# Performance work log

Measured on AMD Instinct MI355X. Metric: run time of the kernel, lower is better.

Reference implementation:

```python
import math
import jax, jax.numpy as jnp
import numpy as np

D_MODEL = 768
D_CROSS = 768
D_HEAD = 64
N_HEADS = D_MODEL // D_HEAD  # 12
D_FF = D_MODEL * 3           # 2304
EPS = 1e-6
N_FREQ = D_HEAD // 8         # freqs per axis (3 axes -> theta dim 24, rotates first 48 of 64 dims)


def make_rope_freqs():
    # k-diffusion style geometric frequencies in [pi, 10*pi), one table shared per head
    n = N_HEADS * N_FREQ
    f = np.exp(np.linspace(math.log(math.pi), math.log(10.0 * math.pi), n + 1)[:-1])
    return jnp.asarray(f.reshape(N_FREQ, N_HEADS).T, dtype=jnp.float32)  # [nh, N_FREQ]

ROPE_FREQS = make_rope_freqs()


def rms_norm(x, scale):
    ms = jnp.mean(jnp.square(x), axis=-1, keepdims=True)
    return x * (scale * jax.lax.rsqrt(ms + EPS))


def cos_scale(q, k, scale):
    # cosine-sim QK rescale: unit-normalize q,k per head then multiply by sqrt(learned scale)
    s = jnp.sqrt(scale)[:, None, None]  # [nh,1,1]
    q = q * (s * jax.lax.rsqrt(jnp.sum(jnp.square(q), -1, keepdims=True) + EPS))
    k = k * (s * jax.lax.rsqrt(jnp.sum(jnp.square(k), -1, keepdims=True) + EPS))
    return q, k


def rope_theta(pos):
    # pos [b,l,3] -> theta [b,nh,l,3*N_FREQ]
    b, l, _ = pos.shape
    th = pos[..., None, :, None] * ROPE_FREQS[:, None, :]  # [b,l,nh,3,N_FREQ]
    th = th.reshape(b, l, N_HEADS, 3 * N_FREQ)
    return jnp.swapaxes(th, 1, 2)  # movedim(-2,-3)


def apply_rope(x, theta):
    d = theta.shape[-1]
    x1, x2, x3 = x[..., :d], x[..., d:2 * d], x[..., 2 * d:]
    c, s = jnp.cos(theta), jnp.sin(theta)
    return jnp.concatenate([x1 * c - x2 * s, x2 * c + x1 * s, x3], axis=-1)


def sdpa(q, k, v):
    # scale=1.0 (cosine-sim already scaled)
    a = jax.nn.softmax(jnp.einsum('bhqe,bhke->bhqk', q, k), axis=-1)
    return jnp.einsum('bhqk,bhke->bhqe', a, v)


def reference(x, pos, x_cross, pos_cross,
              sa_norm_scale, sa_wqkv, sa_scale, sa_wout,
              ca_norm_scale, ca_norm_cross_scale, ca_wq, ca_wkv, ca_scale, ca_wout,
              ff_norm_scale, ff_wup, ff_wdown):
    b, l, _ = x.shape
    lc = x_cross.shape[1]

    # --- self attention ---
    h = rms_norm(x, sa_norm_scale)
    qkv = (h @ sa_wqkv.T).reshape(b, l, 3, N_HEADS, D_HEAD).transpose(2, 0, 3, 1, 4)
    q, k, v = qkv[0], qkv[1], qkv[2]  # [b,nh,l,e]
    q, k = cos_scale(q, k, sa_scale)
    theta = rope_theta(pos)
    q = apply_rope(q, theta)
    k = apply_rope(k, theta)
    o = sdpa(q, k, v)
    o = jnp.swapaxes(o, 1, 2).reshape(b, l, D_MODEL)
    x = o @ sa_wout.T + x

    # --- cross attention ---
    h = rms_norm(x, ca_norm_scale)
    hc = rms_norm(x_cross, ca_norm_cross_scale)
    q = (h @ ca_wq.T).reshape(b, l, N_HEADS, D_HEAD).transpose(0, 2, 1, 3)
    kv = (hc @ ca_wkv.T).reshape(b, lc, 2, N_HEADS, D_HEAD).transpose(2, 0, 3, 1, 4)
    k, v = kv[0], kv[1]
    q, k = cos_scale(q, k, ca_scale)
    q = apply_rope(q, rope_theta(pos))
    k = apply_rope(k, rope_theta(pos_cross))
    o = sdpa(q, k, v)
    o = jnp.swapaxes(o, 1, 2).reshape(b, l, D_MODEL)
    x = o @ ca_wout.T + x

    # --- SwiGLU FFN ---
    u = rms_norm(x, ff_norm_scale) @ ff_wup.T  # [b,l,2*d_ff]
    a, g = jnp.split(u, 2, axis=-1)
    x = (a * jax.nn.silu(g)) @ ff_wdown.T + x
    return x


def setup_inputs() -> dict:
    key = jax.random.key(0)
    ks = jax.random.split(key, 16)
    B, L = 2, 2048

    def w(k, out_f, in_f):
        return jax.random.normal(k, (out_f, in_f), dtype=jnp.float32) * (1.0 / math.sqrt(in_f))

    return {
        'x': jax.random.normal(ks[0], (B, L, D_MODEL), dtype=jnp.float32),
        'pos': jax.random.uniform(ks[1], (B, L, 3), dtype=jnp.float32),
        'x_cross': jax.random.normal(ks[2], (B, L, D_CROSS), dtype=jnp.float32),
        'pos_cross': jax.random.uniform(ks[3], (B, L, 3), dtype=jnp.float32),
        'sa_norm_scale': jnp.ones((D_MODEL,), jnp.float32),
        'sa_wqkv': w(ks[4], 3 * D_MODEL, D_MODEL),
        'sa_scale': jnp.full((N_HEADS,), 10.0, jnp.float32),
        'sa_wout': w(ks[5], D_MODEL, D_MODEL) * 0.02,
        'ca_norm_scale': jnp.ones((D_MODEL,), jnp.float32),
        'ca_norm_cross_scale': jnp.ones((D_CROSS,), jnp.float32),
        'ca_wq': w(ks[6], D_MODEL, D_MODEL),
        'ca_wkv': w(ks[7], 2 * D_MODEL, D_CROSS),
        'ca_scale': jnp.full((N_HEADS,), 10.0, jnp.float32),
        'ca_wout': w(ks[8], D_MODEL, D_MODEL) * 0.02,
        'ff_norm_scale': jnp.ones((D_MODEL,), jnp.float32),
        'ff_wup': w(ks[9], 2 * D_FF, D_MODEL),
        'ff_wdown': w(ks[10], D_MODEL, D_FF) * 0.02,
    }
```

## Files before the change

### kernel.cpp

```cpp
#include <hip/hip_runtime.h>
#include <hip/hip_bf16.h>
#include <math.h>

typedef __hip_bfloat16 bf16;

#define B 2
#define L 2048
#define DM 768
#define NH 12
#define DH 64
#define DFF 2304
#define M_TOK (B * L)

typedef __attribute__((ext_vector_type(8))) short bfrag;
typedef __attribute__((ext_vector_type(4))) float ffrag;
typedef __attribute__((ext_vector_type(16))) float facc16;

__device__ __forceinline__ float waveSum(float v) {
#pragma unroll
  for (int o = 32; o > 0; o >>= 1) v += __shfl_down(v, o, 64);
  return v;
}

__device__ __forceinline__ void gld16(void* l, const void* g) {
  __builtin_amdgcn_global_load_lds((const __attribute__((address_space(1))) unsigned*)g,
                                   (__attribute__((address_space(3))) unsigned*)l, 16, 0, 0);
}

#define BAR1_N(N) do { asm volatile("s_waitcnt vmcnt(" #N ")" ::: "memory"); \
                       __builtin_amdgcn_s_barrier(); } while (0)
#define BAR2() do { asm volatile("s_waitcnt lgkmcnt(0)" ::: "memory"); \
                    __builtin_amdgcn_s_barrier(); } while (0)

#define ASW(row, chunk) (((row) << 6) + ((((chunk) ^ ((row)&7))) << 3))

__global__ void k_castall(const float* __restrict__ s0, const float* __restrict__ s1,
                          const float* __restrict__ s2, const float* __restrict__ s3,
                          const float* __restrict__ s4, const float* __restrict__ s5,
                          const float* __restrict__ s6, bf16* __restrict__ dst) {
  const size_t DM2 = (size_t)DM * DM;
  size_t u = ((size_t)blockIdx.x * 256 + threadIdx.x) * 4;
  if (u >= 17 * DM2) return;
  const float* src;
  size_t loc;
  if (u < 3 * DM2) { src = s0; loc = u; }
  else if (u < 4 * DM2) { src = s1; loc = u - 3 * DM2; }
  else if (u < 5 * DM2) { src = s2; loc = u - 4 * DM2; }
  else if (u < 7 * DM2) { src = s3; loc = u - 5 * DM2; }
  else if (u < 8 * DM2) { src = s4; loc = u - 7 * DM2; }
  else if (u < 14 * DM2) { src = s5; loc = u - 8 * DM2; }
  else { src = s6; loc = u - 14 * DM2; }
  float4 v = *(const float4*)&src[loc];
  bf16* d = dst + u;
  d[0] = __float2bfloat16(v.x);
  d[1] = __float2bfloat16(v.y);
  d[2] = __float2bfloat16(v.z);
  d[3] = __float2bfloat16(v.w);
}

__global__ __launch_bounds__(256) void k_rmsnorm(const float* __restrict__ in,
                                                 const float* __restrict__ scale,
                                                 bf16* __restrict__ out) {
  int row = blockIdx.x;
  int t = threadIdx.x;
  const float* r = in + (size_t)row * DM;
  float x0 = r[t], x1 = r[t + 256], x2 = r[t + 512];
  float ss = x0 * x0 + x1 * x1 + x2 * x2;
  ss = waveSum(ss);
  __shared__ float red[4];
  int w = t >> 6, ln = t & 63;
  if (ln == 0) red[w] = ss;
  __syncthreads();
  float tot = red[0] + red[1] + red[2] + red[3];
  float g = rsqrtf(tot / (float)DM + 1e-6f);
  bf16* o = out + (size_t)row * DM;
  o[t] = __float2bfloat16(x0 * g * scale[t]);
  o[t + 256] = __float2bfloat16(x1 * g * scale[t + 256]);
  o[t + 512] = __float2bfloat16(x2 * g * scale[t + 512]);
}

template <int NT, int OBF>
__global__ __launch_bounds__(256) void k_gemm(const bf16* __restrict__ A,
                                              const bf16* __restrict__ W,
                                              float* __restrict__ C,
                                              bf16* __restrict__ Cb,
                                              const float* __restrict__ res,
                                              int M, int N, int K) {
  __shared__ __align__(16) bf16 As[2 * 128 * 32];
  __shared__ __align__(16) bf16 Bs[2 * NT * 32];
  const int t = threadIdx.x;
  const int w = t >> 6, lane = t & 63;
  const int m0 = blockIdx.y * 128, n0 = blockIdx.x * NT;
  const int quad = lane >> 4, l16 = lane & 15;
  constexpr int MI = (NT == 128) ? 4 : 2;
  const int wrow = (NT == 128) ? (w >> 1) * 64 : w * 32;
  const int wcol = (NT == 128) ? (w & 1) * 64 : 0;

  ffrag acc[MI][4];
#pragma unroll
  for (int i = 0; i < MI; i++)
#pragma unroll
    for (int j = 0; j < 4; j++) acc[i][j] = (ffrag){0.f, 0.f, 0.f, 0.f};

  auto stage = [&](int k0, int sel) {
#pragma unroll
    for (int it = 0; it < 2; it++) {
      int lc = (w * 2 + it) * 64 + lane;
      int row = lc >> 2;
      int kc = (lc & 3) ^ ((row >> 1) & 3);
      gld16(&As[sel * 4096 + lc * 8], &A[(size_t)(m0 + row) * K + k0 + kc * 8]);
    }
    if (NT == 128) {
#pragma unroll
      for (int it = 0; it < 2; it++) {
        int lc = (w * 2 + it) * 64 + lane;
        int row = lc >> 2;
        int kc = (lc & 3) ^ ((row >> 1) & 3);
        gld16(&Bs[sel * 4096 + lc * 8], &W[(size_t)(n0 + row) * K + k0 + kc * 8]);
      }
    } else {
      int lc = w * 64 + lane;
      int row = lc >> 2;
      int kc = (lc & 3) ^ ((row >> 1) & 3);
      gld16(&Bs[sel * 2048 + lc * 8], &W[(size_t)(n0 + row) * K + k0 + kc * 8]);
    }
  };

  const int NK = K >> 5;
  stage(0, 0);
  for (int kt = 0; kt < NK; kt++) {
    int cur = kt & 1;
    if (kt + 1 < NK) {
      stage((kt + 1) * 32, cur ^ 1);
      if constexpr (NT == 128) BAR1_N(4); else BAR1_N(3);
    } else {
      BAR1_N(0);
    }
    const bf16* Ab = As + cur * 4096;
    const bf16* Bb = Bs + cur * (NT == 128 ? 4096 : 2048);
    bfrag af[MI], bfv[4];
#pragma unroll
    for (int i = 0; i < MI; i++) {
      int r = wrow + i * 16 + l16;
      af[i] = *(const bfrag*)&Ab[r * 32 + (quad ^ ((r >> 1) & 3)) * 8];
    }
#pragma unroll
    for (int j = 0; j < 4; j++) {
      int r = wcol + j * 16 + l16;
      bfv[j] = *(const bfrag*)&Bb[r * 32 + (quad ^ ((r >> 1) & 3)) * 8];
    }
#pragma unroll
    for (int i = 0; i < MI; i++)
#pragma unroll
      for (int j = 0; j < 4; j++)
        acc[i][j] = __builtin_amdgcn_mfma_f32_16x16x32_bf16(af[i], bfv[j], acc[i][j], 0, 0, 0);
    BAR2();
  }
#pragma unroll
  for (int i = 0; i < MI; i++) {
    int mrow = m0 + wrow + i * 16 + quad * 4;
#pragma unroll
    for (int j = 0; j < 4; j++) {
      int ncol = n0 + wcol + j * 16 + l16;
#pragma unroll
      for (int r = 0; r < 4; r++) {
        float v = acc[i][j][r];
        size_t idx = (size_t)(mrow + r) * N + ncol;
        if (OBF) {
          Cb[idx] = __float2bfloat16(v);
        } else {
          if (res) v += res[idx];
          C[idx] = v;
        }
      }
    }
  }
}

__global__ __launch_bounds__(256) void k_ffup(const bf16* __restrict__ A,
                                              const bf16* __restrict__ Wup,
                                              bf16* __restrict__ Out) {
  __shared__ __align__(16) bf16 As[2 * 128 * 32];
  __shared__ __align__(16) bf16 Ba[2 * 64 * 32];
  __shared__ __align__(16) bf16 Bg[2 * 64 * 32];
  const int t = threadIdx.x, w = t >> 6, lane = t & 63;
  const int m0 = blockIdx.y * 128, n0 = blockIdx.x * 64;
  const int quad = lane >> 4, l16 = lane & 15;

  ffrag aa[2][4], ag[2][4];
#pragma unroll
  for (int i = 0; i < 2; i++)
#pragma unroll
    for (int j = 0; j < 4; j++) {
      aa[i][j] = (ffrag){0.f, 0.f, 0.f, 0.f};
      ag[i][j] = (ffrag){0.f, 0.f, 0.f, 0.f};
    }

  auto stage = [&](int k0, int sel) {
#pragma unroll
    for (int it = 0; it < 2; it++) {
      int lc = (w * 2 + it) * 64 + lane;
      int row = lc >> 2;
      int kc = (lc & 3) ^ ((row >> 1) & 3);
      gld16(&As[sel * 4096 + lc * 8], &A[(size_t)(m0 + row) * DM + k0 + kc * 8]);
    }
    {
      int lc = w * 64 + lane;
      int row = lc >> 2;
      int kc = (lc & 3) ^ ((row >> 1) & 3);
      gld16(&Ba[sel * 2048 + lc * 8], &Wup[(size_t)(n0 + row) * DM + k0 + kc * 8]);
      gld16(&Bg[sel * 2048 + lc * 8], &Wup[(size_t)(DFF + n0 + row) * DM + k0 + kc * 8]);
    }
  };

  const int NK = DM / 32;
  stage(0, 0);
  for (int kt = 0; kt < NK; kt++) {
    int cur = kt & 1;
    if (kt + 1 < NK) {
      stage((kt + 1) * 32, cur ^ 1);
      BAR1_N(4);
    } else {
      BAR1_N(0);
    }
    const bf16* Ab = As + cur * 4096;
    const bf16* Bab = Ba + cur * 2048;
    const bf16* Bgb = Bg + cur * 2048;
    bfrag af[2], ba[4], bg[4];
#pragma unroll
    for (int i = 0; i < 2; i++) {
      int r = w * 32 + i * 16 + l16;
      af[i] = *(const bfrag*)&Ab[r * 32 + (quad ^ ((r >> 1) & 3)) * 8];
    }
#pragma unroll
    for (int j = 0; j < 4; j++) {
      int r = j * 16 + l16;
      int sw = (quad ^ ((r >> 1) & 3)) * 8;
      ba[j] = *(const bfrag*)&Bab[r * 32 + sw];
      bg[j] = *(const bfrag*)&Bgb[r * 32 + sw];
    }
#pragma unroll
    for (int i = 0; i < 2; i++)
#pragma unroll
      for (int j = 0; j < 4; j++) {
        aa[i][j] = __builtin_amdgcn_mfma_f32_16x16x32_bf16(af[i], ba[j], aa[i][j], 0, 0, 0);
        ag[i][j] = __builtin_amdgcn_mfma_f32_16x16x32_bf16(af[i], bg[j], ag[i][j], 0, 0, 0);
      }
    BAR2();
  }
#pragma unroll
  for (int i = 0; i < 2; i++) {
    int mrow = m0 + w * 32 + i * 16 + quad * 4;
#pragma unroll
    for (int j = 0; j < 4; j++) {
      int ncol = n0 + j * 16 + l16;
#pragma unroll
      for (int r = 0; r < 4; r++) {
        float a = aa[i][j][r], g = ag[i][j][r];
        float v = a * g / (1.f + __expf(-g));
        Out[(size_t)(mrow + r) * DFF + ncol] = __float2bfloat16(v);
      }
    }
  }
}

__device__ __forceinline__ float rope_apply(float x, const float* __restrict__ pos3, float s,
                                            int h, int lane) {
  float ss = x * x;
#pragma unroll
  for (int m = 32; m > 0; m >>= 1) ss += __shfl_xor(ss, m, 64);
  x *= s * rsqrtf(ss + 1e-6f);
  int j = lane < 24 ? lane : (lane < 48 ? lane - 24 : 0);
  int partner = lane < 24 ? lane + 24 : (lane < 48 ? lane - 24 : lane);
  float other = __shfl(x, partner, 64);
  if (lane < 48) {
    int c = j >> 3, f = j & 7;
    float fr = __expf(1.14472988584940017f +
                      (float)(f * 12 + h) * (2.30258509299404568f / 96.0f));
    float th = pos3[c] * fr;
    float st = __sinf(th), ct = __cosf(th);
    return (lane < 24) ? (x * ct - other * st) : (x * ct + other * st);
  }
  return x;
}

__global__ __launch_bounds__(256) void k_ropeqk(const bf16* __restrict__ inQ, int strQ, int offQ,
                                                const bf16* __restrict__ inK, int strK, int offK,
                                                const float* __restrict__ posQ,
                                                const float* __restrict__ posK,
                                                const float* __restrict__ scale,
                                                bf16* __restrict__ outQ, bf16* __restrict__ outK) {
  int item = blockIdx.x * 4 + (threadIdx.x >> 6);
  int lane = threadIdx.x & 63;
  int l = item % L;
  int bh = item / L;
  int h = bh % NH;
  int b = bh / NH;
  float s = sqrtf(scale[h]);
  size_t tokrow = (size_t)(b * L + l);
  float xq = __bfloat162float(inQ[tokrow * strQ + offQ + h * DH + lane]);
  float oq = rope_apply(xq, &posQ[tokrow * 3], s, h, lane);
  outQ[(size_t)item * DH + lane] = __float2bfloat16(oq);
  float xk = __bfloat162float(inK[tokrow * strK + offK + h * DH + lane]);
  float ok = rope_apply(xk, &posK[tokrow * 3], s, h, lane);
  outK[(size_t)item * DH + lane] = __float2bfloat16(ok);
}

__global__ __launch_bounds__(256) void k_vtrans(const bf16* __restrict__ in, int stride, int off,
                                                bf16* __restrict__ Vt) {
  __shared__ __align__(16) bf16 St[64 * 64];
  int lt = blockIdx.x & 31, bh = blockIdx.x >> 5;
  int h = bh % NH, b = bh / NH;
  int t = threadIdx.x;
#pragma unroll
  for (int pass = 0; pass < 2; pass++) {
    int cid = t + pass * 256;
    int r = cid >> 3, c = cid & 7;
    *(float4*)&St[ASW(r, c)] =
        *(const float4*)&in[(size_t)(b * L + lt * 64 + r) * stride + off + h * DH + c * 8];
  }
  __syncthreads();
  const short* Ss = (const short*)St;
#pragma unroll
  for (int pass = 0; pass < 2; pass++) {
    int cid = t + pass * 256;
    int d = cid >> 3, oc = cid & 7;
    bfrag tmp;
#pragma unroll
    for (int i = 0; i < 8; i++) {
      int p = oc * 8 + i;
      int tok = (p & ~12) | ((p & 4) << 1) | ((p & 8) >> 1);
      tmp[i] = Ss[(tok << 6) + ((((d >> 3) ^ (tok & 7))) << 3) + (d & 7)];
    }
    *(bfrag*)&Vt[((size_t)bh * DH + d) * L + lt * 64 + oc * 8] = tmp;
  }
}

__global__ __launch_bounds__(256) void k_attn_mfma(const bf16* __restrict__ Q,
                                                   const bf16* __restrict__ K,
                                                   const bf16* __restrict__ Vt,
                                                   const float* __restrict__ scale,
                                                   bf16* __restrict__ O) {
  __shared__ __align__(16) char smem[32768 + 512];
  bf16* Ks = (bf16*)smem;
  bf16* Vs = (bf16*)(smem + 16384);
  float* Oex = (float*)smem;
  float* Lred = (float*)(smem + 32768);
  int qt = blockIdx.x & 31, bh = blockIdx.x >> 5;
  int h = bh % NH, b = bh / NH;
  float smax = scale[h];
  float nsl2 = -smax * 1.442695040888963f;
  int t = threadIdx.x, w = t >> 6, lane = t & 63;
  int hh = lane >> 5, l32 = lane & 31;
  int qsub = w >> 1, ksub = w & 1;

  const bf16* kbase = K + (size_t)(bh * L) * DH;
  const bf16* vbase = Vt + (size_t)bh * DH * L;

  const bf16* qrow = Q + ((size_t)(bh * L) + qt * 64 + qsub * 32 + l32) * DH;
  bfrag qf[4];
#pragma unroll
  for (int c = 0; c < 4; c++) qf[c] = *(const bfrag*)&qrow[c * 16 + hh * 8];

  facc16 o0, o1;
#pragma unroll
  for (int i = 0; i < 16; i++) { o0[i] = 0.f; o1[i] = 0.f; }
  float l_run = 0.f;

  auto stageKV = [&](int kt, int sel) {
    int k0 = kt * 64;
    bf16* Kb = Ks + sel * 4096;
    bf16* Vb = Vs + sel * 4096;
#pragma unroll
    for (int h2 = 0; h2 < 2; h2++) {
      int r = w * 8 + (lane >> 3) + h2 * 32;
      int kc = (lane & 7) ^ (r & 7);
      int ldsrow = (w * 8 + h2 * 32) * 64;
      gld16(&Kb[ldsrow + lane * 8], &kbase[(size_t)(k0 + r) * DH + kc * 8]);
      gld16(&Vb[ldsrow + lane * 8], &vbase[(size_t)r * L + k0 + kc * 8]);
    }
  };

  stageKV(0, 0);
  for (int kt = 0; kt < 32; kt++) {
    int cur = kt & 1;
    if (kt < 31) {
      stageKV(kt + 1, cur ^ 1);
      BAR1_N(4);
    } else {
      BAR1_N(0);
    }
    const bf16* Kb = Ks + cur * 4096;
    const bf16* Vb = Vs + cur * 4096;
    facc16 s;
#pragma unroll
    for (int i = 0; i < 16; i++) s[i] = 0.f;
#pragma unroll
    for (int c = 0; c < 4; c++) {
      bfrag kf = *(const bfrag*)&Kb[ASW(ksub * 32 + l32, c * 2 + hh)];
      s = __builtin_amdgcn_mfma_f32_32x32x16_bf16(kf, qf[c], s, 0, 0, 0);
    }
    float pv[16];
#pragma unroll
    for (int reg = 0; reg < 16; reg++) {
      float p = __builtin_amdgcn_exp2f(__builtin_fmaf(s[reg], 1.442695040888963f, nsl2));
      l_run += p;
      pv[reg] = p;
    }
    bfrag pf0, pf1;
#pragma unroll
    for (int j = 0; j < 8; j++) {
      pf0[j] = __builtin_bit_cast(short, __float2bfloat16(pv[j]));
      pf1[j] = __builtin_bit_cast(short, __float2bfloat16(pv[8 + j]));
    }
    {
      bfrag vf;
      vf = *(const bfrag*)&Vb[ASW(l32, ksub * 4 + hh)];
      o0 = __builtin_amdgcn_mfma_f32_32x32x16_bf16(pf0, vf, o0, 0, 0, 0);
      vf = *(const bfrag*)&Vb[ASW(l32, ksub * 4 + 2 + hh)];
      o0 = __builtin_amdgcn_mfma_f32_32x32x16_bf16(pf1, vf, o0, 0, 0, 0);
      vf = *(const bfrag*)&Vb[ASW(32 + l32, ksub * 4 + hh)];
      o1 = __builtin_amdgcn_mfma_f32_32x32x16_bf16(pf0, vf, o1, 0, 0, 0);
      vf = *(const bfrag*)&Vb[ASW(32 + l32, ksub * 4 + 2 + hh)];
      o1 = __builtin_amdgcn_mfma_f32_32x32x16_bf16(pf1, vf, o1, 0, 0, 0);
    }
    BAR2();
  }
  l_run += __shfl_xor(l_run, 32, 64);
  __syncthreads();
  {
    int gd = (ksub ^ 1) * 32 + l32;
#pragma unroll
    for (int reg = 0; reg < 16; reg++) {
      int row = (reg & 3) + 8 * (reg >> 2) + 4 * hh;
      float gv = ksub ? o0[reg] : o1[reg];
      Oex[(size_t)(qsub * 32 + row) * 64 + gd] = gv;
    }
  }
  if (lane < 32) Lred[ksub * 64 + qsub * 32 + lane] = l_run;
  __syncthreads();
  {
    int d = ksub * 32 + l32;
#pragma unroll
    for (int reg = 0; reg < 16; reg++) {
      int row = (reg & 3) + 8 * (reg >> 2) + 4 * hh;
      int qg2 = qsub * 32 + row;
      float ltot = Lred[qg2] + Lred[64 + qg2];
      float keep = ksub ? o1[reg] : o0[reg];
      float v = (keep + Oex[(size_t)qg2 * 64 + d]) / ltot;
      O[(((size_t)(b * L) + qt * 64 + qg2) * NH + h) * DH + d] = __float2bfloat16(v);
    }
  }
}

extern "C" void kernel_launch(void* const* d_in, const int* in_sizes, int n_in,
                              void* d_out, int out_size, void* d_ws, size_t ws_size,
                              hipStream_t stream) {
  const float* x = (const float*)d_in[0];
  const float* pos = (const float*)d_in[1];
  const float* x_cross = (const float*)d_in[2];
  const float* pos_cross = (const float*)d_in[3];
  const float* sa_norm_scale = (const float*)d_in[4];
  const float* sa_wqkv = (const float*)d_in[5];
  const float* sa_scale = (const float*)d_in[6];
  const float* sa_wout = (const float*)d_in[7];
  const float* ca_norm_scale = (const float*)d_in[8];
  const float* ca_norm_cross_scale = (const float*)d_in[9];
  const float* ca_wq = (const float*)d_in[10];
  const float* ca_wkv = (const float*)d_in[11];
  const float* ca_scale = (const float*)d_in[12];
  const float* ca_wout = (const float*)d_in[13];
  const float* ff_norm_scale = (const float*)d_in[14];
  const float* ff_wup = (const float*)d_in[15];
  const float* ff_wdown = (const float*)d_in[16];
  float* out = (float*)d_out;

  float* ws = (float*)d_ws;
  const size_t S = (size_t)M_TOK * DM;
  float* xbuf = ws;
  bf16* b16 = (bf16*)(ws + S);
  bf16* qkvb = b16;
  bf16* qb = b16 + 3 * S;
  bf16* kb = b16 + 4 * S;
  bf16* vtb = b16 + 5 * S;
  bf16* hb = b16 + 6 * S;
  bf16* hcb = b16 + 7 * S;
  bf16* obb = b16 + 8 * S;
  bf16* wqkvb = b16 + 9 * S;
  bf16* woutb = wqkvb + (size_t)3 * DM * DM;
  bf16* wqb = woutb + (size_t)DM * DM;
  bf16* wkvb = wqb + (size_t)DM * DM;
  bf16* wout2b = wkvb + (size_t)2 * DM * DM;
  bf16* wupb = wout2b + (size_t)DM * DM;
  bf16* wdownb = wupb + (size_t)2 * DFF * DM;
  bf16* ffb = qkvb;

  const int ropeGrid = B * NH * L / 4;
  const int attnGrid = B * NH * (L / 64);
  const int vtGrid = B * NH * (L / 64);
  const size_t DM2 = (size_t)DM * DM;
  const int castGrid = (int)((17 * DM2 / 4 + 255) / 256);

  k_castall<<<castGrid, 256, 0, stream>>>(sa_wqkv, sa_wout, ca_wq, ca_wkv, ca_wout, ff_wup,
                                          ff_wdown, wqkvb);

  k_rmsnorm<<<M_TOK, 256, 0, stream>>>(x_cross, ca_norm_cross_scale, hcb);

  k_rmsnorm<<<M_TOK, 256, 0, stream>>>(x, sa_norm_scale, hb);
  k_gemm<128, 1><<<dim3(3 * DM / 128, M_TOK / 128), 256, 0, stream>>>(
      hb, wqkvb, nullptr, qkvb, nullptr, M_TOK, 3 * DM, DM);
  k_ropeqk<<<ropeGrid, 256, 0, stream>>>(qkvb, 3 * DM, 0, qkvb, 3 * DM, DM, pos, pos, sa_scale,
                                         qb, kb);
  k_vtrans<<<vtGrid, 256, 0, stream>>>(qkvb, 3 * DM, 2 * DM, vtb);
  k_attn_mfma<<<attnGrid, 256, 0, stream>>>(qb, kb, vtb, sa_scale, obb);
  k_gemm<64, 0><<<dim3(DM / 64, M_TOK / 128), 256, 0, stream>>>(
      obb, woutb, xbuf, nullptr, x, M_TOK, DM, DM);

  k_rmsnorm<<<M_TOK, 256, 0, stream>>>(xbuf, ca_norm_scale, hb);
  k_gemm<64, 1><<<dim3(DM / 64, M_TOK / 128), 256, 0, stream>>>(
      hb, wqb, nullptr, qkvb, nullptr, M_TOK, DM, DM);
  k_gemm<128, 1><<<dim3(2 * DM / 128, M_TOK / 128), 256, 0, stream>>>(
      hcb, wkvb, nullptr, qkvb + S, nullptr, M_TOK, 2 * DM, DM);
  k_ropeqk<<<ropeGrid, 256, 0, stream>>>(qkvb, DM, 0, qkvb + S, 2 * DM, 0, pos, pos_cross,
                                         ca_scale, qb, kb);
  k_vtrans<<<vtGrid, 256, 0, stream>>>(qkvb + S, 2 * DM, DM, vtb);
  k_attn_mfma<<<attnGrid, 256, 0, stream>>>(qb, kb, vtb, ca_scale, obb);
  k_gemm<64, 0><<<dim3(DM / 64, M_TOK / 128), 256, 0, stream>>>(
      obb, wout2b, xbuf, nullptr, xbuf, M_TOK, DM, DM);

  k_rmsnorm<<<M_TOK, 256, 0, stream>>>(xbuf, ff_norm_scale, hb);
  k_ffup<<<dim3(DFF / 64, M_TOK / 128), 256, 0, stream>>>(hb, wupb, ffb);
  k_gemm<64, 0><<<dim3(DM / 64, M_TOK / 128), 256, 0, stream>>>(
      ffb, wdownb, out, nullptr, xbuf, M_TOK, DM, DFF);
}
```

Baseline: 459.5 us.

## Vectorize RoPE to 8 lanes per head row and precompute load pointers

The RoPE/cos-scale kernel now processes each head row with 8 lanes handling 8 bf16 elements each, using 128-bit loads and stores and a 3-step shuffle reduction. Per-element exp-based frequencies are replaced by a geometric recurrence, and the grid shrinks 8x. Separately, the GEMM, SwiGLU GEMM and attention staging lambdas precompute global pointers and LDS offsets once and advance the pointers each k-step, cutting per-iteration address arithmetic. The frequency recurrence can accumulate small rounding differences compared with computing each frequency directly.

```diff
diff --git a/kernel.cpp b/kernel.cpp
--- a/kernel.cpp
+++ b/kernel.cpp
@@ -102,36 +102,41 @@
 #pragma unroll
     for (int j = 0; j < 4; j++) acc[i][j] = (ffrag){0.f, 0.f, 0.f, 0.f};
 
-  auto stage = [&](int k0, int sel) {
-#pragma unroll
-    for (int it = 0; it < 2; it++) {
-      int lc = (w * 2 + it) * 64 + lane;
-      int row = lc >> 2;
-      int kc = (lc & 3) ^ ((row >> 1) & 3);
-      gld16(&As[sel * 4096 + lc * 8], &A[(size_t)(m0 + row) * K + k0 + kc * 8]);
-    }
+  const bf16 *pA0, *pA1, *pB0, *pB1 = nullptr;
+  int lA0, lA1, lB0, lB1 = 0;
+  {
+    int lc0 = (w * 2 + 0) * 64 + lane;
+    int r0 = lc0 >> 2, kc0 = (lc0 & 3) ^ ((r0 >> 1) & 3);
+    int lc1 = (w * 2 + 1) * 64 + lane;
+    int r1 = lc1 >> 2, kc1 = (lc1 & 3) ^ ((r1 >> 1) & 3);
+    pA0 = A + (size_t)(m0 + r0) * K + kc0 * 8; lA0 = lc0 * 8;
+    pA1 = A + (size_t)(m0 + r1) * K + kc1 * 8; lA1 = lc1 * 8;
     if (NT == 128) {
-#pragma unroll
-      for (int it = 0; it < 2; it++) {
-        int lc = (w * 2 + it) * 64 + lane;
-        int row = lc >> 2;
-        int kc = (lc & 3) ^ ((row >> 1) & 3);
-        gld16(&Bs[sel * 4096 + lc * 8], &W[(size_t)(n0 + row) * K + k0 + kc * 8]);
-      }
+      pB0 = W + (size_t)(n0 + r0) * K + kc0 * 8; lB0 = lc0 * 8;
+      pB1 = W + (size_t)(n0 + r1) * K + kc1 * 8; lB1 = lc1 * 8;
     } else {
       int lc = w * 64 + lane;
-      int row = lc >> 2;
-      int kc = (lc & 3) ^ ((row >> 1) & 3);
-      gld16(&Bs[sel * 2048 + lc * 8], &W[(size_t)(n0 + row) * K + k0 + kc * 8]);
+      int r = lc >> 2, kc = (lc & 3) ^ ((r >> 1) & 3);
+      pB0 = W + (size_t)(n0 + r) * K + kc * 8; lB0 = lc * 8;
+    }
+  }
+  auto stage = [&](int sel) {
+    gld16(&As[sel * 4096 + lA0], pA0); pA0 += 32;
+    gld16(&As[sel * 4096 + lA1], pA1); pA1 += 32;
+    if (NT == 128) {
+      gld16(&Bs[sel * 4096 + lB0], pB0); pB0 += 32;
+      gld16(&Bs[sel * 4096 + lB1], pB1); pB1 += 32;
+    } else {
+      gld16(&Bs[sel * 2048 + lB0], pB0); pB0 += 32;
     }
   };
 
   const int NK = K >> 5;
-  stage(0, 0);
+  stage(0);
   for (int kt = 0; kt < NK; kt++) {
     int cur = kt & 1;
     if (kt + 1 < NK) {
-      stage((kt + 1) * 32, cur ^ 1);
+      stage(cur ^ 1);
       if constexpr (NT == 128) BAR1_N(4); else BAR1_N(3);
     } else {
       BAR1_N(0);
@@ -196,29 +201,34 @@
       ag[i][j] = (ffrag){0.f, 0.f, 0.f, 0.f};
     }
 
-  auto stage = [&](int k0, int sel) {
-#pragma unroll
-    for (int it = 0; it < 2; it++) {
-      int lc = (w * 2 + it) * 64 + lane;
-      int row = lc >> 2;
-      int kc = (lc & 3) ^ ((row >> 1) & 3);
-      gld16(&As[sel * 4096 + lc * 8], &A[(size_t)(m0 + row) * DM + k0 + kc * 8]);
-    }
-    {
-      int lc = w * 64 + lane;
-      int row = lc >> 2;
-      int kc = (lc & 3) ^ ((row >> 1) & 3);
-      gld16(&Ba[sel * 2048 + lc * 8], &Wup[(size_t)(n0 + row) * DM + k0 + kc * 8]);
-      gld16(&Bg[sel * 2048 + lc * 8], &Wup[(size_t)(DFF + n0 + row) * DM + k0 + kc * 8]);
-    }
+  const bf16 *pA0, *pA1, *pBa, *pBg;
+  int lA0, lA1, lBc;
+  {
+    int lc0 = (w * 2 + 0) * 64 + lane;
+    int r0 = lc0 >> 2, kc0 = (lc0 & 3) ^ ((r0 >> 1) & 3);
+    int lc1 = (w * 2 + 1) * 64 + lane;
+    int r1 = lc1 >> 2, kc1 = (lc1 & 3) ^ ((r1 >> 1) & 3);
+    pA0 = A + (size_t)(m0 + r0) * DM + kc0 * 8; lA0 = lc0 * 8;
+    pA1 = A + (size_t)(m0 + r1) * DM + kc1 * 8; lA1 = lc1 * 8;
+    int lc = w * 64 + lane;
+    int r = lc >> 2, kc = (lc & 3) ^ ((r >> 1) & 3);
+    pBa = Wup + (size_t)(n0 + r) * DM + kc * 8;
+    pBg = Wup + (size_t)(DFF + n0 + r) * DM + kc * 8;
+    lBc = lc * 8;
+  }
+  auto stage = [&](int sel) {
+    gld16(&As[sel * 4096 + lA0], pA0); pA0 += 32;
+    gld16(&As[sel * 4096 + lA1], pA1); pA1 += 32;
+    gld16(&Ba[sel * 2048 + lBc], pBa); pBa += 32;
+    gld16(&Bg[sel * 2048 + lBc], pBg); pBg += 32;
   };
 
   const int NK = DM / 32;
-  stage(0, 0);
+  stage(0);
   for (int kt = 0; kt < NK; kt++) {
     int cur = kt & 1;
     if (kt + 1 < NK) {
-      stage((kt + 1) * 32, cur ^ 1);
+      stage(cur ^ 1);
       BAR1_N(4);
     } else {
       BAR1_N(0);
@@ -264,24 +274,45 @@
   }
 }
 
-__device__ __forceinline__ float rope_apply(float x, const float* __restrict__ pos3, float s,
-                                            int h, int lane) {
-  float ss = x * x;
-#pragma unroll
-  for (int m = 32; m > 0; m >>= 1) ss += __shfl_xor(ss, m, 64);
-  x *= s * rsqrtf(ss + 1e-6f);
-  int j = lane < 24 ? lane : (lane < 48 ? lane - 24 : 0);
-  int partner = lane < 24 ? lane + 24 : (lane < 48 ? lane - 24 : lane);
-  float other = __shfl(x, partner, 64);
-  if (lane < 48) {
-    int c = j >> 3, f = j & 7;
-    float fr = __expf(1.14472988584940017f +
-                      (float)(f * 12 + h) * (2.30258509299404568f / 96.0f));
-    float th = pos3[c] * fr;
-    float st = __sinf(th), ct = __cosf(th);
-    return (lane < 24) ? (x * ct - other * st) : (x * ct + other * st);
-  }
-  return x;
+__device__ __forceinline__ void rope8(const bf16* __restrict__ inp, const float* __restrict__ pos3,
+                                      float s, float fr0, int k, int lane,
+                                      bf16* __restrict__ outp) {
+  bfrag v = *(const bfrag*)inp;
+  float x[8];
+#pragma unroll
+  for (int i = 0; i < 8; i++) x[i] = __bfloat162float(__builtin_bit_cast(bf16, (short)v[i]));
+  float ss = 0.f;
+#pragma unroll
+  for (int i = 0; i < 8; i++) ss += x[i] * x[i];
+  ss += __shfl_xor(ss, 1, 64);
+  ss += __shfl_xor(ss, 2, 64);
+  ss += __shfl_xor(ss, 4, 64);
+  float g = s * rsqrtf(ss + 1e-6f);
+#pragma unroll
+  for (int i = 0; i < 8; i++) x[i] *= g;
+  int pk = k < 3 ? k + 3 : (k < 6 ? k - 3 : k);
+  int psrc = (lane & 56) | pk;
+  float other[8];
+#pragma unroll
+  for (int i = 0; i < 8; i++) other[i] = __shfl(x[i], psrc, 64);
+  bfrag o;
+  if (k < 6) {
+    int c = k < 3 ? k : k - 3;
+    float p = pos3[c];
+    float fr = fr0;
+    float sgn = k < 3 ? -1.f : 1.f;
+#pragma unroll
+    for (int i = 0; i < 8; i++) {
+      float th = p * fr;
+      fr *= 1.333521432163324f;
+      float st = __sinf(th), ct = __cosf(th);
+      o[i] = __builtin_bit_cast(short, __float2bfloat16(x[i] * ct + sgn * other[i] * st));
+    }
+  } else {
+#pragma unroll
+    for (int i = 0; i < 8; i++) o[i] = __builtin_bit_cast(short, __float2bfloat16(x[i]));
+  }
+  *(bfrag*)outp = o;
 }
 
 __global__ __launch_bounds__(256) void k_ropeqk(const bf16* __restrict__ inQ, int strQ, int offQ,
@@ -290,20 +321,21 @@
                                                 const float* __restrict__ posK,
                                                 const float* __restrict__ scale,
                                                 bf16* __restrict__ outQ, bf16* __restrict__ outK) {
-  int item = blockIdx.x * 4 + (threadIdx.x >> 6);
+  int wid = blockIdx.x * 4 + (threadIdx.x >> 6);
   int lane = threadIdx.x & 63;
+  int k = lane & 7;
+  int item = wid * 8 + (lane >> 3);
   int l = item % L;
   int bh = item / L;
   int h = bh % NH;
   int b = bh / NH;
   float s = sqrtf(scale[h]);
+  float fr0 = __expf(1.14472988584940017f + (float)h * 0.023985261385354646f);
   size_t tokrow = (size_t)(b * L + l);
-  float xq = __bfloat162float(inQ[tokrow * strQ + offQ + h * DH + lane]);
-  float oq = rope_apply(xq, &posQ[tokrow * 3], s, h, lane);
-  outQ[(size_t)item * DH + lane] = __float2bfloat16(oq);
-  float xk = __bfloat162float(inK[tokrow * strK + offK + h * DH + lane]);
-  float ok = rope_apply(xk, &posK[tokrow * 3], s, h, lane);
-  outK[(size_t)item * DH + lane] = __float2bfloat16(ok);
+  rope8(inQ + tokrow * strQ + offQ + h * DH + k * 8, &posQ[tokrow * 3], s, fr0, k, lane,
+        outQ + (size_t)item * DH + k * 8);
+  rope8(inK + tokrow * strK + offK + h * DH + k * 8, &posK[tokrow * 3], s, fr0, k, lane,
+        outK + (size_t)item * DH + k * 8);
 }
 
 __global__ __launch_bounds__(256) void k_vtrans(const bf16* __restrict__ in, int stride, int off,
@@ -367,25 +399,32 @@
   for (int i = 0; i < 16; i++) { o0[i] = 0.f; o1[i] = 0.f; }
   float l_run = 0.f;
 
-  auto stageKV = [&](int kt, int sel) {
-    int k0 = kt * 64;
-    bf16* Kb = Ks + sel * 4096;
-    bf16* Vb = Vs + sel * 4096;
-#pragma unroll
-    for (int h2 = 0; h2 < 2; h2++) {
-      int r = w * 8 + (lane >> 3) + h2 * 32;
-      int kc = (lane & 7) ^ (r & 7);
-      int ldsrow = (w * 8 + h2 * 32) * 64;
-      gld16(&Kb[ldsrow + lane * 8], &kbase[(size_t)(k0 + r) * DH + kc * 8]);
-      gld16(&Vb[ldsrow + lane * 8], &vbase[(size_t)r * L + k0 + kc * 8]);
-    }
+  const bf16 *kg0, *kg1, *vg0, *vg1;
+  int lk0, lk1;
+  {
+    int r0 = w * 8 + (lane >> 3);
+    int kc0 = (lane & 7) ^ (r0 & 7);
+    int r1 = r0 + 32;
+    int kc1 = (lane & 7) ^ (r1 & 7);
+    kg0 = kbase + (size_t)r0 * DH + kc0 * 8;
+    kg1 = kbase + (size_t)r1 * DH + kc1 * 8;
+    vg0 = vbase + (size_t)r0 * L + kc0 * 8;
+    vg1 = vbase + (size_t)r1 * L + kc1 * 8;
+    lk0 = (w * 8) * 64 + lane * 8;
+    lk1 = (w * 8 + 32) * 64 + lane * 8;
+  }
+  auto stageKV = [&](int sel) {
+    gld16(&Ks[sel * 4096 + lk0], kg0); kg0 += 64 * DH;
+    gld16(&Ks[sel * 4096 + lk1], kg1); kg1 += 64 * DH;
+    gld16(&Vs[sel * 4096 + lk0], vg0); vg0 += 64;
+    gld16(&Vs[sel * 4096 + lk1], vg1); vg1 += 64;
   };
 
-  stageKV(0, 0);
+  stageKV(0);
   for (int kt = 0; kt < 32; kt++) {
     int cur = kt & 1;
     if (kt < 31) {
-      stageKV(kt + 1, cur ^ 1);
+      stageKV(cur ^ 1);
       BAR1_N(4);
     } else {
       BAR1_N(0);
@@ -495,7 +534,7 @@
   bf16* wdownb = wupb + (size_t)2 * DFF * DM;
   bf16* ffb = qkvb;
 
-  const int ropeGrid = B * NH * L / 4;
+  const int ropeGrid = B * NH * L / 32;
   const int attnGrid = B * NH * (L / 64);
   const int vtGrid = B * NH * (L / 64);
   const size_t DM2 = (size_t)DM * DM;
```

New measurement: 448.3 us. 2.4% less time.
